# Optimization experiments

Hardware: AMD Instinct MI355X
Metric: run time of the kernel (lower is better)

Reference implementation:

```python
import jax, jax.numpy as jnp
import numpy as np

B, S, D = 2, 2048, 1024
H, DH = 16, 64  # n_heads, d_head = d_model // n_heads


def setup_inputs() -> dict:
    key = jax.random.key(0)
    ks = jax.random.split(key, 8)
    sc = lambda d: 1.0 / np.sqrt(d)
    return {
        "x": jax.random.normal(ks[0], (B, S, D), jnp.float32),
        "context": jax.random.normal(ks[1], (B, D), jnp.float32),
        "prev_state": jax.random.normal(ks[2], (B, S, D), jnp.float32),
        "attention_mask": jnp.ones((B, 1, S, S), dtype=bool),
        "Wq": jax.random.normal(ks[3], (D, D), jnp.float32) * sc(D),
        "Wk": jax.random.normal(ks[4], (D, D), jnp.float32) * sc(D),
        "Wv": jax.random.normal(ks[5], (D, D), jnp.float32) * sc(D),
        "Wo": jax.random.normal(ks[6], (D, D), jnp.float32) * sc(D),
        "Wc": jax.random.normal(ks[7], (D, DH), jnp.float32) * sc(D),
        "alpha": jnp.ones((1,), jnp.float32),
        "beta": jnp.ones((1,), jnp.float32),
    }


def reference(x, context, prev_state, attention_mask, Wq, Wk, Wv, Wo, Wc, alpha, beta):
    b, s, d = x.shape
    # projections (Linear with no bias, weight stored as [out, in] -> x @ W.T)
    q = (x @ Wq.T).reshape(b, s, H, DH).transpose(0, 2, 1, 3)  # (B,H,S,DH)
    k = (x @ Wk.T).reshape(b, s, H, DH).transpose(0, 2, 1, 3)
    v = (x @ Wv.T).reshape(b, s, H, DH).transpose(0, 2, 1, 3)

    inv_sqrt_dh = 1.0 / jnp.sqrt(jnp.asarray(DH, x.dtype))
    scores = jnp.einsum("bhqd,bhkd->bhqk", q, k) * inv_sqrt_dh

    # CFM: context-flow matching bias, rank-1 per-pair term from global context
    c = context @ Wc  # (B, DH)
    qc = jnp.einsum("bhqd,bd->bhq", q, c)
    kc = jnp.einsum("bhkd,bd->bhk", k, c)
    cfm = qc[..., :, None] * kc[..., None, :] / DH  # (B,H,S,S)

    # AFM: anti-flow matching bias from previous layer state (first d_head dims)
    p = prev_state[..., :DH]  # (B,S,DH)
    afm = jnp.einsum("bhqd,bkd->bhqk", q, p) * inv_sqrt_dh

    scores = scores + alpha[0] * cfm - beta[0] * afm
    scores = jnp.where(attention_mask, scores, jnp.asarray(-1e9, scores.dtype))

    w = jax.nn.softmax(scores, axis=-1)
    out = jnp.einsum("bhqk,bhkd->bhqd", w, v)  # (B,H,S,DH)
    out = out.transpose(0, 2, 1, 3).reshape(b, s, d)
    return out @ Wo.T
```

## Files before the change

kernel.cpp:

```cpp
#include <hip/hip_runtime.h>
#include <stdint.h>

#define D_  1024
#define S_  2048
#define B_  2
#define H_  16
#define DH_ 64
#define M_  (B_*S_)

typedef __bf16 bf16x8 __attribute__((ext_vector_type(8)));
typedef float  f32x4  __attribute__((ext_vector_type(4)));
typedef short  short8 __attribute__((ext_vector_type(8)));
typedef unsigned short u16;

static __device__ __forceinline__ u16 f2bf(float f){
  union { float f; unsigned u; } v; v.f = f;
  unsigned r = v.u + 0x7FFF + ((v.u >> 16) & 1);
  return (u16)(r >> 16);
}
static __device__ __forceinline__ f32x4 mfma16(short8 a, short8 b, f32x4 c){
  return __builtin_amdgcn_mfma_f32_16x16x32_bf16(
      __builtin_bit_cast(bf16x8, a), __builtin_bit_cast(bf16x8, b), c, 0, 0, 0);
}
static __device__ __forceinline__ float fexp2(float x){
#if __has_builtin(__builtin_amdgcn_exp2f)
  return __builtin_amdgcn_exp2f(x);
#else
  return __exp2f(x);
#endif
}
static __device__ __forceinline__ void gl_lds16(const u16* g, u16* lds){
  __builtin_amdgcn_global_load_lds(
      (const __attribute__((address_space(1))) void*)(uintptr_t)g,
      (__attribute__((address_space(3))) void*)(uintptr_t)lds, 16, 0, 0);
}

__global__ void k_f2bf(const float* __restrict__ in, u16* __restrict__ out, int n4){
  int i = blockIdx.x * blockDim.x + threadIdx.x;
  if(i >= n4) return;
  float4 v = ((const float4*)in)[i];
  ushort4 o; o.x = f2bf(v.x); o.y = f2bf(v.y); o.z = f2bf(v.z); o.w = f2bf(v.w);
  ((ushort4*)out)[i] = o;
}

__global__ void k_f2bf4(const float* __restrict__ a0, const float* __restrict__ a1,
                        const float* __restrict__ a2, const float* __restrict__ a3,
                        u16* __restrict__ o0, u16* __restrict__ o1,
                        u16* __restrict__ o2, u16* __restrict__ o3, int n4){
  const float* in; u16* out;
  switch(blockIdx.y){
    case 0: in=a0; out=o0; break;
    case 1: in=a1; out=o1; break;
    case 2: in=a2; out=o2; break;
    default: in=a3; out=o3; break;
  }
  int i = blockIdx.x * blockDim.x + threadIdx.x;
  if(i >= n4) return;
  float4 v = ((const float4*)in)[i];
  ushort4 o; o.x = f2bf(v.x); o.y = f2bf(v.y); o.z = f2bf(v.z); o.w = f2bf(v.w);
  ((ushort4*)out)[i] = o;
}

__global__ void k_ctx(const float* __restrict__ context, const float* __restrict__ Wc,
                      float* __restrict__ cvec, int* __restrict__ flags){
  __shared__ float partial[4][2][64];
  int t = threadIdx.x;
  if(t < 2) flags[t] = 1;
  int c = t >> 7;
  int b = (t >> 6) & 1;
  int j = t & 63;
  float s = 0.f;
  #pragma unroll 8
  for(int d = c*256; d < (c+1)*256; ++d) s += context[b*D_ + d] * Wc[d*DH_ + j];
  partial[c][b][j] = s;
  __syncthreads();
  if(t < 128){
    int b2 = t >> 6, j2 = t & 63;
    cvec[b2*DH_ + j2] = partial[0][b2][j2] + partial[1][b2][j2]
                      + partial[2][b2][j2] + partial[3][b2][j2];
  }
}

__global__ void k_mask_check(const uint4* __restrict__ m, int n16, int* flags){
  int i = blockIdx.x * blockDim.x + threadIdx.x;
  bool ok8 = true, ok32 = true;
  if(i < n16){
    uint4 v = m[i];
    ok8  = (v.x==0x01010101u)&&(v.y==0x01010101u)&&(v.z==0x01010101u)&&(v.w==0x01010101u);
    ok32 = (v.x==1u)&&(v.y==1u)&&(v.z==1u)&&(v.w==1u);
  }
  unsigned long long b8  = __ballot(!ok8);
  unsigned long long b32 = __ballot(!ok32);
  if((threadIdx.x & 63) == 0){
    if(b8)  flags[0] = 0;
    if(b32) flags[1] = 0;
  }
}

template<int MODE>
__global__ __launch_bounds__(256,2) void k_gemm(const u16* __restrict__ A, const u16* __restrict__ W,
                                                void* __restrict__ Cout,
                                                const float* __restrict__ cvec,
                                                const float* __restrict__ prev,
                                                const float* __restrict__ beta_p,
                                                float* __restrict__ qkc){
  __shared__ u16 As[128*64];
  __shared__ u16 Bs[64*64];
  __shared__ float red[2][2][64];
  const int tid = threadIdx.x;
  const int w = tid >> 6, l = tid & 63;
  const int wr = w >> 1, wc = w & 1;
  const int bm = blockIdx.x >> 4;
  const int bn = blockIdx.x & 15;
  const int lr = l & 15, lh = l >> 4;
  const int srow = l >> 3, scol = (l & 7) * 8;

  f32x4 acc[4][2] = {};

  for(int kt = 0; kt < 16; ++kt){
    const int k0 = kt * 64;
    #pragma unroll
    for(int i = 0; i < 4; ++i){
      const int chunk = i*4 + w;
      const u16* ga = A + (size_t)(bm*128 + chunk*8 + srow)*D_ + k0 + scol;
      gl_lds16(ga, &As[chunk*512]);
    }
    #pragma unroll
    for(int i = 0; i < 2; ++i){
      const int chunk = w*2 + i;
      const u16* gb = W + (size_t)(bn*64 + chunk*8 + srow)*D_ + k0 + scol;
      gl_lds16(gb, &Bs[chunk*512]);
    }
    __syncthreads();
    #pragma unroll
    for(int kk = 0; kk < 2; ++kk){
      short8 a[4], b[2];
      #pragma unroll
      for(int m = 0; m < 4; ++m)
        a[m] = *(const short8*)&As[(wr*64 + m*16 + lr)*64 + kk*32 + lh*8];
      #pragma unroll
      for(int n = 0; n < 2; ++n)
        b[n] = *(const short8*)&Bs[(wc*32 + n*16 + lr)*64 + kk*32 + lh*8];
      #pragma unroll
      for(int m = 0; m < 4; ++m)
        #pragma unroll
        for(int n = 0; n < 2; ++n)
          acc[m][n] = mfma16(a[m], b[n], acc[m][n]);
    }
    __syncthreads();
  }

  const int b = bm >> 4;

  if constexpr (MODE <= 1){
    const float cv0 = cvec[b*DH_ + wc*32 + lr];
    const float cv1 = cvec[b*DH_ + wc*32 + 16 + lr];
    float part[4][4];
    #pragma unroll
    for(int m = 0; m < 4; ++m)
      #pragma unroll
      for(int r = 0; r < 4; ++r){
        float p = acc[m][0][r]*cv0 + acc[m][1][r]*cv1;
        p += __shfl_xor(p, 1, 64); p += __shfl_xor(p, 2, 64);
        p += __shfl_xor(p, 4, 64); p += __shfl_xor(p, 8, 64);
        part[m][r] = p;
      }
    if(lr == 0){
      #pragma unroll
      for(int m = 0; m < 4; ++m)
        #pragma unroll
        for(int r = 0; r < 4; ++r)
          red[wr][wc][m*16 + lh*4 + r] = part[m][r];
    }
    __syncthreads();
    if(tid < 128){
      int wr2 = tid >> 6, i = tid & 63;
      float v = red[wr2][0][i] + red[wr2][1][i];
      int s = (bm & 15)*128 + wr2*64 + i;
      qkc[((size_t)b*H_ + bn)*S_ + s] = v;
    }
  }

  if constexpr (MODE == 1){
    const float beta = beta_p[0];
    #pragma unroll
    for(int m = 0; m < 4; ++m)
      #pragma unroll
      for(int n = 0; n < 2; ++n)
        #pragma unroll
        for(int r = 0; r < 4; ++r){
          size_t row = (size_t)bm*128 + wr*64 + m*16 + lh*4 + r;
          acc[m][n][r] -= beta * prev[row*D_ + wc*32 + n*16 + lr];
        }
  }

  if constexpr (MODE == 2){
    #pragma unroll
    for(int m = 0; m < 4; ++m){
      const int s0 = (bm & 15)*128 + wr*64 + m*16 + lh*4;
      #pragma unroll
      for(int n = 0; n < 2; ++n){
        const int col = bn*64 + wc*32 + n*16 + lr;
        ushort4 o;
        o.x = f2bf(acc[m][n][0]); o.y = f2bf(acc[m][n][1]);
        o.z = f2bf(acc[m][n][2]); o.w = f2bf(acc[m][n][3]);
        *(ushort4*)&((u16*)Cout)[((size_t)(b*1024 + col))*S_ + s0] = o;
      }
    }
  } else {
    #pragma unroll
    for(int m = 0; m < 4; ++m){
      const size_t row0 = (size_t)bm*128 + wr*64 + m*16 + lh*4;
      #pragma unroll
      for(int n = 0; n < 2; ++n){
        const size_t col = (size_t)bn*64 + wc*32 + n*16 + lr;
        #pragma unroll
        for(int r = 0; r < 4; ++r){
          if constexpr (MODE == 3) ((float*)Cout)[(row0 + r)*D_ + col] = acc[m][n][r];
          else                     ((u16*)Cout)[(row0 + r)*D_ + col] = f2bf(acc[m][n][r]);
        }
      }
    }
  }
}

__global__ __launch_bounds__(256,2) void k_attn(const u16* __restrict__ Qb,
    const u16* __restrict__ Kb, const u16* __restrict__ VT,
    const float* __restrict__ qc, const float* __restrict__ kc,
    const float* __restrict__ alpha_p, const unsigned char* __restrict__ mask,
    const int* __restrict__ flags, u16* __restrict__ Ob){
  __shared__ u16 Kbuf[2][4096];
  __shared__ u16 Vbuf[2][4096];
  __shared__ u16 Ps[4][32*72];
  const int tid = threadIdx.x;
  const int w = tid >> 6, l = tid & 63;
  const int lr = l & 15, lh = l >> 4;
  const int id = blockIdx.x;
  const int bh = id & 31, qb = id >> 5;
  const int b = bh >> 4, h = bh & 15;
  const int q0 = qb*128 + w*32;
  const float LOG2E = 1.44269504088896340736f;
  const float s1 = 0.125f * LOG2E;
  const float aL = alpha_p[0] * (1.0f/64.0f) * LOG2E;
  const bool allones = (flags[0] | flags[1]) != 0;
  const u16* Kb_h = Kb + (size_t)b*S_*D_ + h*DH_;
  const u16* VT_h = VT + ((size_t)(b*1024 + h*DH_))*S_;
  const float* kcp = kc + (size_t)bh*S_;
  const unsigned char* maskb = mask + (size_t)b*S_*S_;
  u16* PsW = &Ps[w][0];

  const int srow = l >> 3;
  const int sdh  = ((l & 7) ^ srow) * 8;
  const int iw0 = w*2, iw1 = w*2 + 1;
  #define STAGEK(TILE, BUF) {                                                  \
    const u16* _p = Kb_h + (size_t)(TILE)*64*D_;                               \
    gl_lds16(_p + (size_t)(iw0*8 + srow)*D_ + sdh, &Kbuf[BUF][iw0*512]);       \
    gl_lds16(_p + (size_t)(iw1*8 + srow)*D_ + sdh, &Kbuf[BUF][iw1*512]); }
  #define STAGEV(TILE, BUF) {                                                  \
    const u16* _p = VT_h + (size_t)(TILE)*64;                                  \
    gl_lds16(_p + (size_t)(iw0*8 + srow)*S_ + sdh, &Vbuf[BUF][iw0*512]);       \
    gl_lds16(_p + (size_t)(iw1*8 + srow)*S_ + sdh, &Vbuf[BUF][iw1*512]); }

  short8 qa[2][2];
  float aq[2][4];
  #pragma unroll
  for(int qi = 0; qi < 2; ++qi){
    const size_t qrow = ((size_t)b*S_ + q0 + qi*16 + lr)*D_ + h*DH_;
    qa[qi][0] = *(const short8*)&Qb[qrow + lh*8];
    qa[qi][1] = *(const short8*)&Qb[qrow + 32 + lh*8];
    #pragma unroll
    for(int j = 0; j < 4; ++j)
      aq[qi][j] = aL * qc[(size_t)bh*S_ + q0 + qi*16 + lh*4 + j];
  }

  f32x4 acc[2][4];
  float lp[2][4];
  #pragma unroll
  for(int qi = 0; qi < 2; ++qi){
    #pragma unroll
    for(int g = 0; g < 4; ++g) acc[qi][g] = (f32x4){0,0,0,0};
    #pragma unroll
    for(int j = 0; j < 4; ++j) lp[qi][j] = 0.f;
  }

  const int rdo0 = lr*64 + ((lh*8)      ^ ((lr & 7) << 3));
  const int rdo1 = lr*64 + ((32 + lh*8) ^ ((lr & 7) << 3));

  float kcv[4], kcn[4];
  #pragma unroll
  for(int cg = 0; cg < 4; ++cg) kcv[cg] = kcp[cg*16 + lr];
  STAGEK(0, 0);
  STAGEV(0, 0);
  __syncthreads();

  for(int kt = 0; kt < 32; ++kt){
    const int buf = kt & 1;
    const int k0 = kt*64;
    const int tn = (kt+1) & 31;
    STAGEK(tn, buf^1);
    STAGEV(tn, buf^1);
    #pragma unroll
    for(int cg = 0; cg < 4; ++cg) kcn[cg] = kcp[tn*64 + cg*16 + lr];

    short8 kb0[4], kb1[4];
    #pragma unroll
    for(int cg = 0; cg < 4; ++cg){
      kb0[cg] = *(const short8*)&Kbuf[buf][cg*1024 + rdo0];
      kb1[cg] = *(const short8*)&Kbuf[buf][cg*1024 + rdo1];
    }
    f32x4 sc[2][4];
    #pragma unroll
    for(int qi = 0; qi < 2; ++qi)
      #pragma unroll
      for(int cg = 0; cg < 4; ++cg){
        sc[qi][cg] = mfma16(qa[qi][0], kb0[cg], (f32x4){0,0,0,0});
        sc[qi][cg] = mfma16(qa[qi][1], kb1[cg], sc[qi][cg]);
      }
    short8 vf0[4], vf1[4];
    #pragma unroll
    for(int g = 0; g < 4; ++g){
      vf0[g] = *(const short8*)&Vbuf[buf][g*1024 + rdo0];
      vf1[g] = *(const short8*)&Vbuf[buf][g*1024 + rdo1];
    }

    #pragma unroll
    for(int qi = 0; qi < 2; ++qi){
      #pragma unroll
      for(int cg = 0; cg < 4; ++cg)
        #pragma unroll
        for(int j = 0; j < 4; ++j){
          float t = sc[qi][cg][j]*s1 + aq[qi][j]*kcv[cg];
          if(!allones){
            unsigned char mm = maskb[((size_t)(q0 + qi*16 + lh*4 + j))*S_ + k0 + cg*16 + lr];
            if(!mm) t = -160.0f;
          }
          float e = fexp2(t);
          lp[qi][j] += e;
          PsW[(qi*16 + lh*4 + j)*72 + cg*16 + lr] = __builtin_bit_cast(u16, (__bf16)e);
        }
      short8 pa0 = *(const short8*)&PsW[(qi*16 + lr)*72 + lh*8];
      short8 pa1 = *(const short8*)&PsW[(qi*16 + lr)*72 + 32 + lh*8];
      #pragma unroll
      for(int g = 0; g < 4; ++g){
        acc[qi][g] = mfma16(pa0, vf0[g], acc[qi][g]);
        acc[qi][g] = mfma16(pa1, vf1[g], acc[qi][g]);
      }
    }
    #pragma unroll
    for(int cg = 0; cg < 4; ++cg) kcv[cg] = kcn[cg];
    __syncthreads();
  }
  #undef STAGEK
  #undef STAGEV

  #pragma unroll
  for(int qi = 0; qi < 2; ++qi){
    float inv[4];
    #pragma unroll
    for(int j = 0; j < 4; ++j){
      float s = lp[qi][j];
      s += __shfl_xor(s, 1, 64); s += __shfl_xor(s, 2, 64);
      s += __shfl_xor(s, 4, 64); s += __shfl_xor(s, 8, 64);
      inv[j] = 1.0f / s;
    }
    #pragma unroll
    for(int g = 0; g < 4; ++g)
      #pragma unroll
      for(int j = 0; j < 4; ++j){
        float o = acc[qi][g][j] * inv[j];
        Ob[((size_t)b*S_ + q0 + qi*16 + lh*4 + j)*D_ + h*DH_ + g*16 + lr] =
          __builtin_bit_cast(u16, (__bf16)o);
      }
  }
}

extern "C" void kernel_launch(void* const* d_in, const int* in_sizes, int n_in,
                              void* d_out, int out_size, void* d_ws, size_t ws_size,
                              hipStream_t stream){
  const float* x    = (const float*)d_in[0];
  const float* ctx  = (const float*)d_in[1];
  const float* prev = (const float*)d_in[2];
  const unsigned char* mask = (const unsigned char*)d_in[3];
  const float* Wq = (const float*)d_in[4];
  const float* Wk = (const float*)d_in[5];
  const float* Wv = (const float*)d_in[6];
  const float* Wo = (const float*)d_in[7];
  const float* Wc = (const float*)d_in[8];
  const float* alpha = (const float*)d_in[9];
  const float* beta  = (const float*)d_in[10];

  char* ws = (char*)d_ws;
  size_t off = 0;
  auto alloc = [&](size_t bytes)->void*{
    void* p = ws + off; off += (bytes + 255) & ~(size_t)255; return p;
  };
  u16* xb  = (u16*)alloc((size_t)M_*D_*2);
  u16* wqb = (u16*)alloc((size_t)D_*D_*2);
  u16* wkb = (u16*)alloc((size_t)D_*D_*2);
  u16* wvb = (u16*)alloc((size_t)D_*D_*2);
  u16* wob = (u16*)alloc((size_t)D_*D_*2);
  u16* Qb  = (u16*)alloc((size_t)M_*D_*2);
  u16* Kb  = (u16*)alloc((size_t)M_*D_*2);
  u16* VT  = (u16*)alloc((size_t)B_*D_*S_*2);
  float* qcb  = (float*)alloc((size_t)B_*H_*S_*4);
  float* kcb  = (float*)alloc((size_t)B_*H_*S_*4);
  float* cvec = (float*)alloc(512);
  int*  flags = (int*)alloc(64);
  u16* Ob = xb;

  k_f2bf<<<M_*D_/4/256, 256, 0, stream>>>(x, xb, M_*D_/4);
  {
    dim3 g(D_*D_/4/256, 4);
    k_f2bf4<<<g, 256, 0, stream>>>(Wq, Wk, Wv, Wo, wqb, wkb, wvb, wob, D_*D_/4);
  }
  k_ctx<<<1, 512, 0, stream>>>(ctx, Wc, cvec, flags);
  {
    int n16 = B_*S_*S_/16;
    k_mask_check<<<n16/256, 256, 0, stream>>>((const uint4*)mask, n16, flags);
  }
  k_gemm<0><<<512, 256, 0, stream>>>(xb, wqb, Qb, cvec, nullptr, nullptr, qcb);
  k_gemm<1><<<512, 256, 0, stream>>>(xb, wkb, Kb, cvec, prev, beta, kcb);
  k_gemm<2><<<512, 256, 0, stream>>>(xb, wvb, VT, cvec, nullptr, nullptr, nullptr);
  k_attn<<<512, 256, 0, stream>>>(Qb, Kb, VT, qcb, kcb, alpha, mask, flags, Ob);
  k_gemm<3><<<512, 256, 0, stream>>>(Ob, wob, d_out, cvec, nullptr, nullptr, nullptr);
}
```

Before: 184.1 us.

## Rewrite attention with 32x32 MFMA, register-resident P via permlane swap

The attention kernel switches from 16x16x32 to 32x32x16 bf16 MFMA, computing S^T = K·Q so each lane owns one query row. Probabilities are packed to bf16 in registers and rearranged with v_permlane32_swap instead of a round trip through LDS, so the P shared buffer goes away. The K-path scale factor is folded into the K projection epilogue, and the launch becomes 1024 blocks of 128 threads. This cuts LDS traffic and the per-element multiply, at the cost of a new block shape that lowers per-block K/V reuse.

```diff
diff --git a/kernel.cpp b/kernel.cpp
--- a/kernel.cpp
+++ b/kernel.cpp
@@ -10,7 +10,9 @@
 
 typedef __bf16 bf16x8 __attribute__((ext_vector_type(8)));
 typedef float  f32x4  __attribute__((ext_vector_type(4)));
+typedef float  f32x16 __attribute__((ext_vector_type(16)));
 typedef short  short8 __attribute__((ext_vector_type(8)));
+typedef unsigned uint4v __attribute__((ext_vector_type(4)));
 typedef unsigned short u16;
 
 static __device__ __forceinline__ u16 f2bf(float f){
@@ -21,6 +23,14 @@
 static __device__ __forceinline__ f32x4 mfma16(short8 a, short8 b, f32x4 c){
   return __builtin_amdgcn_mfma_f32_16x16x32_bf16(
       __builtin_bit_cast(bf16x8, a), __builtin_bit_cast(bf16x8, b), c, 0, 0, 0);
+}
+static __device__ __forceinline__ f32x16 mfma32(short8 a, short8 b, f32x16 c){
+  return __builtin_amdgcn_mfma_f32_32x32x16_bf16(
+      __builtin_bit_cast(bf16x8, a), __builtin_bit_cast(bf16x8, b), c, 0, 0, 0);
+}
+static __device__ __forceinline__ f32x16 zero16(){
+  f32x16 z = {0,0,0,0,0,0,0,0,0,0,0,0,0,0,0,0};
+  return z;
 }
 static __device__ __forceinline__ float fexp2(float x){
 #if __has_builtin(__builtin_amdgcn_exp2f)
@@ -28,6 +38,11 @@
 #else
   return __exp2f(x);
 #endif
+}
+static __device__ __forceinline__ unsigned cvtpk(float lo, float hi){
+  unsigned r;
+  asm("v_cvt_pk_bf16_f32 %0, %1, %2" : "=v"(r) : "v"(lo), "v"(hi));
+  return r;
 }
 static __device__ __forceinline__ void gl_lds16(const u16* g, u16* lds){
   __builtin_amdgcn_global_load_lds(
@@ -183,6 +198,7 @@
 
   if constexpr (MODE == 1){
     const float beta = beta_p[0];
+    const float KSCALE = 0.125f * 1.44269504088896340736f;
     #pragma unroll
     for(int m = 0; m < 4; ++m)
       #pragma unroll
@@ -190,7 +206,7 @@
         #pragma unroll
         for(int r = 0; r < 4; ++r){
           size_t row = (size_t)bm*128 + wr*64 + m*16 + lh*4 + r;
-          acc[m][n][r] -= beta * prev[row*D_ + wc*32 + n*16 + lr];
+          acc[m][n][r] = (acc[m][n][r] - beta * prev[row*D_ + wc*32 + n*16 + lr]) * KSCALE;
         }
   }
 
@@ -224,71 +240,48 @@
   }
 }
 
-__global__ __launch_bounds__(256,2) void k_attn(const u16* __restrict__ Qb,
+__global__ __launch_bounds__(128,2) void k_attn(const u16* __restrict__ Qb,
     const u16* __restrict__ Kb, const u16* __restrict__ VT,
     const float* __restrict__ qc, const float* __restrict__ kc,
     const float* __restrict__ alpha_p, const unsigned char* __restrict__ mask,
     const int* __restrict__ flags, u16* __restrict__ Ob){
   __shared__ u16 Kbuf[2][4096];
   __shared__ u16 Vbuf[2][4096];
-  __shared__ u16 Ps[4][32*72];
   const int tid = threadIdx.x;
-  const int w = tid >> 6, l = tid & 63;
-  const int lr = l & 15, lh = l >> 4;
+  const int wv = tid >> 6, l = tid & 63;
+  const int q32 = l & 31, hi = l >> 5, hb = hi*8;
   const int id = blockIdx.x;
   const int bh = id & 31, qb = id >> 5;
   const int b = bh >> 4, h = bh & 15;
-  const int q0 = qb*128 + w*32;
-  const float LOG2E = 1.44269504088896340736f;
-  const float s1 = 0.125f * LOG2E;
-  const float aL = alpha_p[0] * (1.0f/64.0f) * LOG2E;
+  const int q0w = qb*64 + wv*32;
+  const float aL = alpha_p[0] * (1.0f/64.0f) * 1.44269504088896340736f;
   const bool allones = (flags[0] | flags[1]) != 0;
   const u16* Kb_h = Kb + (size_t)b*S_*D_ + h*DH_;
   const u16* VT_h = VT + ((size_t)(b*1024 + h*DH_))*S_;
   const float* kcp = kc + (size_t)bh*S_;
-  const unsigned char* maskb = mask + (size_t)b*S_*S_;
-  u16* PsW = &Ps[w][0];
+  const unsigned char* maskr = mask + ((size_t)b*S_ + q0w + q32)*S_;
 
   const int srow = l >> 3;
   const int sdh  = ((l & 7) ^ srow) * 8;
-  const int iw0 = w*2, iw1 = w*2 + 1;
-  #define STAGEK(TILE, BUF) {                                                  \
-    const u16* _p = Kb_h + (size_t)(TILE)*64*D_;                               \
-    gl_lds16(_p + (size_t)(iw0*8 + srow)*D_ + sdh, &Kbuf[BUF][iw0*512]);       \
-    gl_lds16(_p + (size_t)(iw1*8 + srow)*D_ + sdh, &Kbuf[BUF][iw1*512]); }
-  #define STAGEV(TILE, BUF) {                                                  \
-    const u16* _p = VT_h + (size_t)(TILE)*64;                                  \
-    gl_lds16(_p + (size_t)(iw0*8 + srow)*S_ + sdh, &Vbuf[BUF][iw0*512]);       \
-    gl_lds16(_p + (size_t)(iw1*8 + srow)*S_ + sdh, &Vbuf[BUF][iw1*512]); }
-
-  short8 qa[2][2];
-  float aq[2][4];
+  #define STAGEK(TILE, BUF) { _Pragma("unroll") for(int j = 0; j < 4; ++j){      \
+      const int ck = j*2 + wv;                                                   \
+      gl_lds16(Kb_h + (size_t)((TILE)*64 + ck*8 + srow)*D_ + sdh,                \
+               &Kbuf[BUF][ck*512]); } }
+  #define STAGEV(TILE, BUF) { _Pragma("unroll") for(int j = 0; j < 4; ++j){      \
+      const int ck = j*2 + wv;                                                   \
+      gl_lds16(VT_h + (size_t)(ck*8 + srow)*S_ + (TILE)*64 + sdh,                \
+               &Vbuf[BUF][ck*512]); } }
+
+  short8 qa[4];
   #pragma unroll
-  for(int qi = 0; qi < 2; ++qi){
-    const size_t qrow = ((size_t)b*S_ + q0 + qi*16 + lr)*D_ + h*DH_;
-    qa[qi][0] = *(const short8*)&Qb[qrow + lh*8];
-    qa[qi][1] = *(const short8*)&Qb[qrow + 32 + lh*8];
-    #pragma unroll
-    for(int j = 0; j < 4; ++j)
-      aq[qi][j] = aL * qc[(size_t)bh*S_ + q0 + qi*16 + lh*4 + j];
-  }
-
-  f32x4 acc[2][4];
-  float lp[2][4];
-  #pragma unroll
-  for(int qi = 0; qi < 2; ++qi){
-    #pragma unroll
-    for(int g = 0; g < 4; ++g) acc[qi][g] = (f32x4){0,0,0,0};
-    #pragma unroll
-    for(int j = 0; j < 4; ++j) lp[qi][j] = 0.f;
-  }
-
-  const int rdo0 = lr*64 + ((lh*8)      ^ ((lr & 7) << 3));
-  const int rdo1 = lr*64 + ((32 + lh*8) ^ ((lr & 7) << 3));
-
-  float kcv[4], kcn[4];
-  #pragma unroll
-  for(int cg = 0; cg < 4; ++cg) kcv[cg] = kcp[cg*16 + lr];
+  for(int c = 0; c < 4; ++c)
+    qa[c] = *(const short8*)&Qb[((size_t)b*S_ + q0w + q32)*D_ + h*DH_ + c*16 + hb];
+  const float aq = aL * qc[(size_t)bh*S_ + q0w + q32];
+
+  f32x16 oacc[2] = {zero16(), zero16()};
+  float lp = 0.f;
+  const int xk = (q32 & 7) << 3;
+
   STAGEK(0, 0);
   STAGEV(0, 0);
   __syncthreads();
@@ -299,79 +292,76 @@
     const int tn = (kt+1) & 31;
     STAGEK(tn, buf^1);
     STAGEV(tn, buf^1);
-    #pragma unroll
-    for(int cg = 0; cg < 4; ++cg) kcn[cg] = kcp[tn*64 + cg*16 + lr];
-
-    short8 kb0[4], kb1[4];
-    #pragma unroll
-    for(int cg = 0; cg < 4; ++cg){
-      kb0[cg] = *(const short8*)&Kbuf[buf][cg*1024 + rdo0];
-      kb1[cg] = *(const short8*)&Kbuf[buf][cg*1024 + rdo1];
-    }
-    f32x4 sc[2][4];
-    #pragma unroll
-    for(int qi = 0; qi < 2; ++qi)
-      #pragma unroll
-      for(int cg = 0; cg < 4; ++cg){
-        sc[qi][cg] = mfma16(qa[qi][0], kb0[cg], (f32x4){0,0,0,0});
-        sc[qi][cg] = mfma16(qa[qi][1], kb1[cg], sc[qi][cg]);
+
+    f32x16 sacc[2] = {zero16(), zero16()};
+    #pragma unroll
+    for(int kg = 0; kg < 2; ++kg)
+      #pragma unroll
+      for(int c = 0; c < 4; ++c){
+        short8 kf = *(const short8*)&Kbuf[buf][(kg*32 + q32)*64 + ((c*16 + hb) ^ xk)];
+        sacc[kg] = mfma32(kf, qa[c], sacc[kg]);
       }
-    short8 vf0[4], vf1[4];
-    #pragma unroll
-    for(int g = 0; g < 4; ++g){
-      vf0[g] = *(const short8*)&Vbuf[buf][g*1024 + rdo0];
-      vf1[g] = *(const short8*)&Vbuf[buf][g*1024 + rdo1];
-    }
-
-    #pragma unroll
-    for(int qi = 0; qi < 2; ++qi){
-      #pragma unroll
-      for(int cg = 0; cg < 4; ++cg)
+    short8 vf[2][4];
+    #pragma unroll
+    for(int dh2 = 0; dh2 < 2; ++dh2)
+      #pragma unroll
+      for(int c = 0; c < 4; ++c)
+        vf[dh2][c] = *(const short8*)&Vbuf[buf][(dh2*32 + q32)*64 + ((c*16 + hb) ^ xk)];
+
+    unsigned pk[2][8];
+    #pragma unroll
+    for(int kg = 0; kg < 2; ++kg){
+      float p[16];
+      #pragma unroll
+      for(int rg = 0; rg < 4; ++rg){
+        f32x4 kv = *(const f32x4*)&kcp[k0 + kg*32 + rg*8 + hi*4];
+        unsigned mu = 0x01010101u;
+        if(!allones) mu = *(const unsigned*)&maskr[k0 + kg*32 + rg*8 + hi*4];
         #pragma unroll
         for(int j = 0; j < 4; ++j){
-          float t = sc[qi][cg][j]*s1 + aq[qi][j]*kcv[cg];
-          if(!allones){
-            unsigned char mm = maskb[((size_t)(q0 + qi*16 + lh*4 + j))*S_ + k0 + cg*16 + lr];
-            if(!mm) t = -160.0f;
-          }
+          float t = sacc[kg][rg*4 + j] + aq*kv[j];
+          if(((mu >> (8*j)) & 255u) == 0u) t = -160.0f;
           float e = fexp2(t);
-          lp[qi][j] += e;
-          PsW[(qi*16 + lh*4 + j)*72 + cg*16 + lr] = __builtin_bit_cast(u16, (__bf16)e);
+          lp += e;
+          p[rg*4 + j] = e;
         }
-      short8 pa0 = *(const short8*)&PsW[(qi*16 + lr)*72 + lh*8];
-      short8 pa1 = *(const short8*)&PsW[(qi*16 + lr)*72 + 32 + lh*8];
-      #pragma unroll
-      for(int g = 0; g < 4; ++g){
-        acc[qi][g] = mfma16(pa0, vf0[g], acc[qi][g]);
-        acc[qi][g] = mfma16(pa1, vf1[g], acc[qi][g]);
       }
-    }
-    #pragma unroll
-    for(int cg = 0; cg < 4; ++cg) kcv[cg] = kcn[cg];
+      #pragma unroll
+      for(int i = 0; i < 8; ++i) pk[kg][i] = cvtpk(p[2*i], p[2*i+1]);
+    }
+
+    #pragma unroll
+    for(int c = 0; c < 4; ++c){
+      const int kg = c >> 1, c4 = (c & 1)*4;
+      unsigned x0 = pk[kg][c4+0], y0 = pk[kg][c4+2];
+      unsigned x1 = pk[kg][c4+1], y1 = pk[kg][c4+3];
+      asm("v_permlane32_swap_b32 %0, %1" : "+v"(x0), "+v"(y0));
+      asm("v_permlane32_swap_b32 %0, %1" : "+v"(x1), "+v"(y1));
+      uint4v pb = {x0, x1, y0, y1};
+      short8 pbf = __builtin_bit_cast(short8, pb);
+      #pragma unroll
+      for(int dh2 = 0; dh2 < 2; ++dh2)
+        oacc[dh2] = mfma32(vf[dh2][c], pbf, oacc[dh2]);
+    }
     __syncthreads();
   }
   #undef STAGEK
   #undef STAGEV
 
+  float lt = lp + __shfl_xor(lp, 32, 64);
+  float inv = 1.0f / lt;
+  u16* orow = Ob + ((size_t)b*S_ + q0w + q32)*D_ + h*DH_;
   #pragma unroll
-  for(int qi = 0; qi < 2; ++qi){
-    float inv[4];
-    #pragma unroll
-    for(int j = 0; j < 4; ++j){
-      float s = lp[qi][j];
-      s += __shfl_xor(s, 1, 64); s += __shfl_xor(s, 2, 64);
-      s += __shfl_xor(s, 4, 64); s += __shfl_xor(s, 8, 64);
-      inv[j] = 1.0f / s;
-    }
-    #pragma unroll
-    for(int g = 0; g < 4; ++g)
-      #pragma unroll
-      for(int j = 0; j < 4; ++j){
-        float o = acc[qi][g][j] * inv[j];
-        Ob[((size_t)b*S_ + q0 + qi*16 + lh*4 + j)*D_ + h*DH_ + g*16 + lr] =
-          __builtin_bit_cast(u16, (__bf16)o);
-      }
-  }
+  for(int dh2 = 0; dh2 < 2; ++dh2)
+    #pragma unroll
+    for(int rg = 0; rg < 4; ++rg){
+      ushort4 o;
+      o.x = f2bf(oacc[dh2][rg*4+0]*inv);
+      o.y = f2bf(oacc[dh2][rg*4+1]*inv);
+      o.z = f2bf(oacc[dh2][rg*4+2]*inv);
+      o.w = f2bf(oacc[dh2][rg*4+3]*inv);
+      *(ushort4*)&orow[dh2*32 + rg*8 + hi*4] = o;
+    }
 }
 
 extern "C" void kernel_launch(void* const* d_in, const int* in_sizes, int n_in,
@@ -421,6 +411,6 @@
   k_gemm<0><<<512, 256, 0, stream>>>(xb, wqb, Qb, cvec, nullptr, nullptr, qcb);
   k_gemm<1><<<512, 256, 0, stream>>>(xb, wkb, Kb, cvec, prev, beta, kcb);
   k_gemm<2><<<512, 256, 0, stream>>>(xb, wvb, VT, cvec, nullptr, nullptr, nullptr);
-  k_attn<<<512, 256, 0, stream>>>(Qb, Kb, VT, qcb, kcb, alpha, mask, flags, Ob);
+  k_attn<<<1024, 128, 0, stream>>>(Qb, Kb, VT, qcb, kcb, alpha, mask, flags, Ob);
   k_gemm<3><<<512, 256, 0, stream>>>(Ob, wob, d_out, cvec, nullptr, nullptr, nullptr);
 }
```

After: 174.2 us. 5.4% less time.
